# Kernel tuning notes

Measured on AMD Instinct MI355X. Metric: run time of the kernel, lower is better.

## Reference

```python
import jax, jax.numpy as jnp
import numpy as np

V, E, H, B, P, Q = 100000, 300, 256, 64, 400, 50
NEG = -1e7


def _gru_param(k, s=0.08):
    k1, k2, k3, k4 = jax.random.split(k, 4)
    return (jax.random.normal(k1, (2, 3 * H, E)) * s,
            jax.random.normal(k2, (2, 3 * H, H)) * s,
            jax.random.normal(k3, (2, 3 * H)) * s,
            jax.random.normal(k4, (2, 3 * H)) * s)


def setup_inputs() -> dict:
    key = jax.random.key(0)
    ks = jax.random.split(key, 10)
    emb = (jax.random.normal(ks[0], (V, E)) * 0.1).at[0].set(0.0)  # padding_idx=0 row zeroed
    passage = jax.random.randint(ks[1], (B, P), 1, V)
    question = jax.random.randint(ks[2], (B, Q), 1, V)
    # variable lengths, padding (token 0) at the tail like pack_padded_sequence assumes
    p_len = 200 + (jnp.arange(B) * 7) % (P - 200)
    q_len = 20 + (jnp.arange(B) * 3) % (Q - 20)
    passage = jnp.where(jnp.arange(P)[None, :] < p_len[:, None], passage, 0)
    question = jnp.where(jnp.arange(Q)[None, :] < q_len[:, None], question, 0)
    pW_ih, pW_hh, pb_ih, pb_hh = _gru_param(ks[3])
    qW_ih, qW_hh, qb_ih, qb_hh = _gru_param(ks[4])
    start_w = jax.random.normal(ks[5], (6 * H,)) * 0.05
    start_b = jax.random.normal(ks[6], ()) * 0.05
    end_w = jax.random.normal(ks[7], (6 * H,)) * 0.05
    end_b = jax.random.normal(ks[8], ()) * 0.05
    return dict(passage=passage, question=question, emb=emb,
                pW_ih=pW_ih, pW_hh=pW_hh, pb_ih=pb_ih, pb_hh=pb_hh,
                qW_ih=qW_ih, qW_hh=qW_hh, qb_ih=qb_ih, qb_hh=qb_hh,
                start_w=start_w, start_b=start_b, end_w=end_w, end_b=end_b)


def bi_gru(x, mask, Wih, Whh, bih, bhh):
    """Bidirectional GRU with packed-sequence-equivalent masking.
    x: (B,T,E), mask: (B,T) float. Returns (B,T,2H). Padded outputs are 0,
    and the backward pass starts at the true last token (mask freezes state)."""
    m = mask[..., None]                                          # (B,T,1)
    xproj = jnp.einsum('bte,dhe->dbth', x, Wih) + bih[:, None, None, :]  # (2,B,T,3H)

    def run(xp, mm, Whh_d, bhh_d):
        def step(h, inp):
            xt, mt = inp                                         # (B,3H),(B,1)
            hp = h @ Whh_d.T + bhh_d
            r = jax.nn.sigmoid(xt[:, :H] + hp[:, :H])
            z = jax.nn.sigmoid(xt[:, H:2 * H] + hp[:, H:2 * H])
            n = jnp.tanh(xt[:, 2 * H:] + r * hp[:, 2 * H:])
            h_new = (1 - z) * n + z * h
            h_new = mt * h_new + (1 - mt) * h
            return h_new, h_new * mt
        h0 = jnp.zeros((xp.shape[0], H), xp.dtype)
        _, out = jax.lax.scan(step, h0, (xp.transpose(1, 0, 2), mm.transpose(1, 0, 2)))
        return out.transpose(1, 0, 2)                            # (B,T,H)

    fwd = run(xproj[0], m, Whh[0], bhh[0])
    bwd = run(xproj[1][:, ::-1], m[:, ::-1], Whh[1], bhh[1])[:, ::-1]
    return jnp.concatenate([fwd, bwd], axis=-1)


def reference(passage, question, emb,
              pW_ih, pW_hh, pb_ih, pb_hh,
              qW_ih, qW_hh, qb_ih, qb_hh,
              start_w, start_b, end_w, end_b):
    p_mask = (passage != 0).astype(jnp.float32)                  # (B,P)
    q_mask = (question != 0).astype(jnp.float32)                 # (B,Q)
    Hp = bi_gru(emb[passage], p_mask, pW_ih, pW_hh, pb_ih, pb_hh)  # (B,P,2H)
    Hq = bi_gru(emb[question], q_mask, qW_ih, qW_hh, qb_ih, qb_hh)  # (B,Q,2H)

    # Trilinear attention: decompose Linear over the cat([p, q, p*q]) terms
    w1, w2, w3 = start_w[:2 * H], start_w[2 * H:4 * H], start_w[4 * H:]
    scores = (Hp @ w1)[:, :, None] + (Hq @ w2)[:, None, :] \
        + jnp.einsum('bpd,bqd->bpq', Hp * w3, Hq) + start_b      # (B,P,Q)

    # allennlp masked_softmax: softmax(vector*mask) * mask, renormalized
    a = jax.nn.softmax(scores * q_mask[:, None, :], axis=-1) * q_mask[:, None, :]
    a = a / (a.sum(axis=-1, keepdims=True) + 1e-13)

    wavg = jnp.einsum('bpq,bqd->bpd', a, Hq)                     # (B,P,2H)
    combined = jnp.concatenate([Hp, wavg, Hp * wavg], axis=-1)   # (B,P,6H)

    start_logits = jnp.where(p_mask > 0, combined @ start_w + start_b, NEG)
    end_logits = jnp.where(p_mask > 0, combined @ end_w + end_b, NEG)
    log_mask = jnp.log(p_mask + 1e-45)
    softmax_start = jax.nn.log_softmax(start_logits + log_mask, axis=-1)
    softmax_end = jax.nn.log_softmax(end_logits + log_mask, axis=-1)
    return start_logits, end_logits, softmax_start, softmax_end
```

## Files before the change

kernel.cpp:

```cpp
#include <hip/hip_runtime.h>
#include <math.h>

constexpr int Bb = 64;
constexpr int Pp = 400;
constexpr int Qq = 50;
constexpr int Ee = 300;
constexpr int Hh = 256;
constexpr int H3 = 768;
constexpr int Dd = 512;

#define NEGC (-10000000.0f)
#define LOGTINY (-103.278929903f)

typedef _Float16 h2 __attribute__((ext_vector_type(2)));
typedef _Float16 f16x8 __attribute__((ext_vector_type(8)));
typedef float f32x4 __attribute__((ext_vector_type(4)));

__device__ __forceinline__ float allred(float v){
  #pragma unroll
  for (int off = 1; off < 64; off <<= 1) v += __shfl_xor(v, off);
  return v;
}
__device__ __forceinline__ float allmax(float v){
  #pragma unroll
  for (int off = 1; off < 64; off <<= 1) v = fmaxf(v, __shfl_xor(v, off));
  return v;
}
__device__ __forceinline__ float sigm(float x){ return 1.f / (1.f + expf(-x)); }

__device__ __forceinline__ float dot2f(unsigned a, unsigned b, float c){
#if __has_builtin(__builtin_amdgcn_fdot2)
  return __builtin_amdgcn_fdot2(__builtin_bit_cast(h2, a), __builtin_bit_cast(h2, b), c, false);
#else
  float r = c;
  asm("v_dot2_f32_f16 %0, %1, %2, %0" : "+v"(r) : "v"(a), "v"(b));
  return r;
#endif
}

#define U4C(v,c) ((c)==0?(v).x:((c)==1?(v).y:((c)==2?(v).z:(v).w)))

__global__ __launch_bounds__(256) void gather_a(const int* __restrict__ ptok,
                                                const int* __restrict__ qtok,
                                                const float* __restrict__ emb,
                                                _Float16* __restrict__ Agp,
                                                _Float16* __restrict__ Agq){
  int idx = blockIdx.x * 256 + threadIdx.x;
  if (idx >= (25600 + 3200) * 40) return;
  int ck = idx % 40;
  int row = idx / 40;
  int tokv; _Float16* dst;
  if (row < 25600){ tokv = ptok[row]; dst = Agp + (size_t)row * 320; }
  else { int r = row - 25600; tokv = qtok[r]; dst = Agq + (size_t)r * 320; }
  int c = ck * 8;
  const float* src = emb + (size_t)tokv * Ee;
  f16x8 v;
  #pragma unroll
  for (int i = 0; i < 8; ++i) v[i] = (c + i < Ee) ? (_Float16)src[c + i] : (_Float16)0.f;
  *(f16x8*)(dst + c) = v;
}

__global__ __launch_bounds__(256) void prep_wih16(const float* __restrict__ pW,
                                                  const float* __restrict__ qW,
                                                  _Float16* __restrict__ wih16){
  int idx = blockIdx.x * 256 + threadIdx.x;
  if (idx >= 2 * 2 * 768 * 160) return;
  int col2 = idx % 160;
  int r = idx / 160;
  int g = r / 1536;
  int dh = r % 1536;
  int c = col2 * 2;
  const float* W = g ? qW : pW;
  float2 v = make_float2(0.f, 0.f);
  if (c < Ee) v = *(const float2*)(W + (size_t)dh * Ee + c);
  h2 o = { (_Float16)v.x, (_Float16)v.y };
  *(h2*)(wih16 + (size_t)r * 320 + c) = o;
}

__global__ __launch_bounds__(256) void prep_w16(const float* __restrict__ pW,
                                                const float* __restrict__ qW,
                                                unsigned* __restrict__ w16){
  int idx = blockIdx.x * 256 + threadIdx.x;
  if (idx >= 393216) return;
  int c = idx & 3;
  int t = (idx >> 2) & 1023;
  int B = idx >> 12;
  int gd, g, ql;
  if (B < 28){
    gd = B / 7; int rb = B % 7;
    ql = rb / 3; g = rb % 3;
  } else if (B < 64){
    int lb0 = B - 28; gd = lb0 / 9; int lb = lb0 % 9;
    if (lb < 2){ ql = 2; g = lb + 1; }
    else if (lb < 8){ int v = lb - 2; ql = 3 + v / 3; g = v % 3; }
    else { ql = 5; g = 0; }
  } else {
    int sb0 = B - 64; gd = sb0 / 8; int sb = sb0 % 8;
    if (sb < 2){ ql = 5; g = sb + 1; }
    else { int v = sb - 2; ql = 6 + v / 3; g = v % 3; }
  }
  int j = t & 255, qq = t >> 8;
  int p = qq * 32 + ql * 4 + c;
  int row = g * 256 + j;
  int d = gd & 1, kind = gd >> 1;
  const float* W = kind ? qW : pW;
  const float* src = W + ((size_t)d * H3 + row) * Hh + 2 * p;
  _Float16 a = (_Float16)src[0], bb = (_Float16)src[1];
  unsigned short ua, ub;
  __builtin_memcpy(&ua, &a, 2); __builtin_memcpy(&ub, &bb, 2);
  w16[idx] = (unsigned)ua | ((unsigned)ub << 16);
}

__global__ __launch_bounds__(512) void xproj_mfma(const _Float16* __restrict__ Ag,
                                                  const _Float16* __restrict__ wih16,
                                                  const float* __restrict__ bih,
                                                  _Float16* __restrict__ xp, int T){
  __shared__ __align__(16) _Float16 Af[128][72];
  __shared__ __align__(16) _Float16 Bf[128][72];
  int tid = threadIdx.x;
  int m0 = blockIdx.y * 128;
  int nt = blockIdx.x;
  int d = nt / 6, h0 = (nt % 6) * 128;
  int wid = tid >> 6, lane = tid & 63;
  int wr = wid >> 2, wc = wid & 3;

  int r0 = tid >> 3;
  int r1 = (tid + 512) >> 3;
  int cc = (tid & 7) * 8;
  const _Float16* eA0 = Ag + (size_t)(m0 + r0) * 320;
  const _Float16* eA1 = Ag + (size_t)(m0 + r1) * 320;
  const _Float16* wB0 = wih16 + ((size_t)d * H3 + h0 + r0) * 320;
  const _Float16* wB1 = wih16 + ((size_t)d * H3 + h0 + r1) * 320;

  f32x4 acc[4][2] = {};

  for (int k0 = 0; k0 < 320; k0 += 64){
    *(f16x8*)&Af[r0][cc] = *(const f16x8*)(eA0 + k0 + cc);
    *(f16x8*)&Af[r1][cc] = *(const f16x8*)(eA1 + k0 + cc);
    *(f16x8*)&Bf[r0][cc] = *(const f16x8*)(wB0 + k0 + cc);
    *(f16x8*)&Bf[r1][cc] = *(const f16x8*)(wB1 + k0 + cc);
    __syncthreads();
    #pragma unroll
    for (int kc = 0; kc < 2; ++kc){
      int kb = kc * 32 + (lane >> 4) * 8;
      f16x8 af[4], bf[2];
      #pragma unroll
      for (int i = 0; i < 4; ++i) af[i] = *(const f16x8*)&Af[wr * 64 + i * 16 + (lane & 15)][kb];
      #pragma unroll
      for (int jn = 0; jn < 2; ++jn) bf[jn] = *(const f16x8*)&Bf[wc * 32 + jn * 16 + (lane & 15)][kb];
      #pragma unroll
      for (int i = 0; i < 4; ++i)
        #pragma unroll
        for (int jn = 0; jn < 2; ++jn)
          acc[i][jn] = __builtin_amdgcn_mfma_f32_16x16x32_f16(af[i], bf[jn], acc[i][jn], 0, 0, 0);
    }
    __syncthreads();
  }

  #pragma unroll
  for (int jn = 0; jn < 2; ++jn){
    int h = h0 + wc * 32 + jn * 16 + (lane & 15);
    float bv = bih[d * H3 + h];
    #pragma unroll
    for (int i = 0; i < 4; ++i){
      #pragma unroll
      for (int r = 0; r < 4; ++r){
        int m = m0 + wr * 64 + i * 16 + (lane >> 4) * 4 + r;
        int bI = m / T, tI = m - bI * T;
        xp[(((size_t)d * Bb + bI) * T + tI) * H3 + h] = (_Float16)(acc[i][jn][r] + bv);
      }
    }
  }
}

__global__ __launch_bounds__(1024)
void gru_kernel(const int* __restrict__ ptok,
                const int* __restrict__ qtok,
                const _Float16* __restrict__ xpp,
                const _Float16* __restrict__ xpq,
                const unsigned* __restrict__ w16,
                const float* __restrict__ pbhh,
                const float* __restrict__ qbhh,
                float* __restrict__ Hp,
                float* __restrict__ Hq){
  int wg = blockIdx.x;
  bool isp = wg < 128;
  int lw = isp ? wg : wg - 128;
  int d = lw & 1, b = lw >> 1;
  int T = isp ? Pp : Qq;
  const int* tok = (isp ? ptok : qtok) + b * T;
  const _Float16* xrow = (isp ? xpp : xpq) + ((size_t)d * Bb + b) * T * H3;
  int gd = (isp ? 0 : 2) + d;
  const float* bhh = (isp ? pbhh : qbhh) + d * H3;
  float* Hout = (isp ? Hp : Hq) + (size_t)b * T * Dd + d * Hh;

  __shared__ __align__(16) uint4 ldsW[9 * 1024];
  __shared__ float part[3][3][Hh];
  __shared__ unsigned hbuf[2][128];

  int t = threadIdx.x;
  int j = t & 255, qq = t >> 8, lane = t & 63;
  const uint4* u4w = (const uint4*)w16;

  unsigned wrR[28];
  #pragma unroll
  for (int rb = 0; rb < 7; ++rb){
    uint4 v = u4w[((size_t)gd * 7 + rb) * 1024 + t];
    wrR[4 * rb + 0] = v.x; wrR[4 * rb + 1] = v.y; wrR[4 * rb + 2] = v.z; wrR[4 * rb + 3] = v.w;
  }
  #pragma unroll
  for (int i = 0; i < 28; ++i) asm volatile("" : "+v"(wrR[i]));

  #pragma unroll
  for (int lb = 0; lb < 9; ++lb)
    ldsW[lb * 1024 + t] = u4w[28 * 1024 + ((size_t)gd * 9 + lb) * 1024 + t];
  const uint4* wS = u4w + 64 * 1024 + (size_t)gd * 8 * 1024;

  float bh0 = bhh[j], bh1 = bhh[Hh + j], bh2 = bhh[2 * Hh + j];
  float h_old = 0.f;
  if (t < 128) hbuf[1][t] = 0u;
  __syncthreads();

  int t0 = d ? (T - 1) : 0;
  float pre0 = 0.f, pre1 = 0.f, pre2 = 0.f;
  if (qq == 0){
    pre0 = (float)xrow[(size_t)t0 * H3 + j];
    pre1 = (float)xrow[(size_t)t0 * H3 + Hh + j];
    pre2 = (float)xrow[(size_t)t0 * H3 + 2 * Hh + j];
  }

  for (int s = 0; s < T; ++s){
    int tt = d ? (T - 1 - s) : s;
    unsigned vh = hbuf[(s + 1) & 1][qq * 32 + (lane & 31)];
    float a0 = 0.f, a1 = 0.f, a2 = 0.f;

    uint4 sA0 = wS[0 * 1024 + t], sA1 = wS[1 * 1024 + t];

    #pragma unroll
    for (int c = 0; c < 4; ++c){
      unsigned hv = (unsigned)__builtin_amdgcn_readlane((int)vh, c);
      a0 = dot2f(wrR[0 + c], hv, a0);
      a1 = dot2f(wrR[4 + c], hv, a1);
      a2 = dot2f(wrR[8 + c], hv, a2);
    }
    #pragma unroll
    for (int c = 0; c < 4; ++c){
      unsigned hv = (unsigned)__builtin_amdgcn_readlane((int)vh, 4 + c);
      a0 = dot2f(wrR[12 + c], hv, a0);
      a1 = dot2f(wrR[16 + c], hv, a1);
      a2 = dot2f(wrR[20 + c], hv, a2);
    }
    #pragma unroll
    for (int c = 0; c < 4; ++c){
      unsigned hv = (unsigned)__builtin_amdgcn_readlane((int)vh, 8 + c);
      a0 = dot2f(wrR[24 + c], hv, a0);
    }

    uint4 sB0 = wS[2 * 1024 + t], sB1 = wS[3 * 1024 + t], sB2 = wS[4 * 1024 + t];

    { uint4 l1 = ldsW[0 * 1024 + t], l2 = ldsW[1 * 1024 + t];
      #pragma unroll
      for (int c = 0; c < 4; ++c){
        unsigned hv = (unsigned)__builtin_amdgcn_readlane((int)vh, 8 + c);
        a1 = dot2f(U4C(l1, c), hv, a1);
        a2 = dot2f(U4C(l2, c), hv, a2);
      } }
    { uint4 l0 = ldsW[2 * 1024 + t], l1 = ldsW[3 * 1024 + t], l2 = ldsW[4 * 1024 + t];
      #pragma unroll
      for (int c = 0; c < 4; ++c){
        unsigned hv = (unsigned)__builtin_amdgcn_readlane((int)vh, 12 + c);
        a0 = dot2f(U4C(l0, c), hv, a0);
        a1 = dot2f(U4C(l1, c), hv, a1);
        a2 = dot2f(U4C(l2, c), hv, a2);
      } }

    #pragma unroll
    for (int c = 0; c < 4; ++c){
      unsigned hv = (unsigned)__builtin_amdgcn_readlane((int)vh, 20 + c);
      a1 = dot2f(U4C(sA0, c), hv, a1);
      a2 = dot2f(U4C(sA1, c), hv, a2);
    }

    uint4 sC0 = wS[5 * 1024 + t], sC1 = wS[6 * 1024 + t], sC2 = wS[7 * 1024 + t];

    { uint4 l0 = ldsW[5 * 1024 + t], l1 = ldsW[6 * 1024 + t], l2 = ldsW[7 * 1024 + t];
      #pragma unroll
      for (int c = 0; c < 4; ++c){
        unsigned hv = (unsigned)__builtin_amdgcn_readlane((int)vh, 16 + c);
        a0 = dot2f(U4C(l0, c), hv, a0);
        a1 = dot2f(U4C(l1, c), hv, a1);
        a2 = dot2f(U4C(l2, c), hv, a2);
      } }
    { uint4 l0 = ldsW[8 * 1024 + t];
      #pragma unroll
      for (int c = 0; c < 4; ++c){
        unsigned hv = (unsigned)__builtin_amdgcn_readlane((int)vh, 20 + c);
        a0 = dot2f(U4C(l0, c), hv, a0);
      } }

    #pragma unroll
    for (int c = 0; c < 4; ++c){
      unsigned hv = (unsigned)__builtin_amdgcn_readlane((int)vh, 24 + c);
      a0 = dot2f(U4C(sB0, c), hv, a0);
      a1 = dot2f(U4C(sB1, c), hv, a1);
      a2 = dot2f(U4C(sB2, c), hv, a2);
    }
    #pragma unroll
    for (int c = 0; c < 4; ++c){
      unsigned hv = (unsigned)__builtin_amdgcn_readlane((int)vh, 28 + c);
      a0 = dot2f(U4C(sC0, c), hv, a0);
      a1 = dot2f(U4C(sC1, c), hv, a1);
      a2 = dot2f(U4C(sC2, c), hv, a2);
    }

    if (qq != 0){
      part[qq - 1][0][j] = a0;
      part[qq - 1][1][j] = a1;
      part[qq - 1][2][j] = a2;
    }
    __syncthreads();
    if (qq == 0){
      float xt0 = pre0, xt1 = pre1, xt2 = pre2;
      if (s + 1 < T){
        int tn = d ? (T - 2 - s) : (s + 1);
        pre0 = (float)xrow[(size_t)tn * H3 + j];
        pre1 = (float)xrow[(size_t)tn * H3 + Hh + j];
        pre2 = (float)xrow[(size_t)tn * H3 + 2 * Hh + j];
      }
      float g0 = a0 + part[0][0][j] + part[1][0][j] + part[2][0][j] + bh0;
      float g1 = a1 + part[0][1][j] + part[1][1][j] + part[2][1][j] + bh1;
      float g2 = a2 + part[0][2][j] + part[1][2][j] + part[2][2][j] + bh2;
      float r = sigm(xt0 + g0);
      float z = sigm(xt1 + g1);
      float n = tanhf(xt2 + r * g2);
      float hnew = (1.f - z) * n + z * h_old;
      float m = (tok[tt] != 0) ? 1.f : 0.f;
      float hm = m * hnew + (1.f - m) * h_old;
      h_old = hm;
      ((_Float16*)hbuf[s & 1])[j] = (_Float16)hm;
      Hout[(size_t)tt * Dd + j] = hm * m;
    }
    __syncthreads();
  }
}

__global__ __launch_bounds__(512) void attn_kernel(const float* __restrict__ Hp,
                                                   const float* __restrict__ Hq,
                                                   const int* __restrict__ ptok,
                                                   const int* __restrict__ qtok,
                                                   const float* __restrict__ start_w,
                                                   const float* __restrict__ sbp,
                                                   const float* __restrict__ end_w,
                                                   const float* __restrict__ ebp,
                                                   float* __restrict__ out){
  extern __shared__ __align__(16) float lds[];
  float* hqs = lds;
  float* s2s = hqs + Qq * Dd;
  float* qms = s2s + 64;
  float* scw = qms + 64;
  float* aw  = scw + 512;

  int b = blockIdx.y, pc = blockIdx.x;
  int tid = threadIdx.x, wid = tid >> 6, lane = tid & 63;
  float sb = sbp[0], eb = ebp[0];

  float w1r[8], w2r[8], w3r[8], e1r[8], e2r[8], e3r[8];
  #pragma unroll
  for (int i = 0; i < 8; ++i){
    int c = lane * 8 + i;
    w1r[i] = start_w[c]; w2r[i] = start_w[Dd + c]; w3r[i] = start_w[2 * Dd + c];
    e1r[i] = end_w[c];   e2r[i] = end_w[Dd + c];   e3r[i] = end_w[2 * Dd + c];
  }
  for (int idx = tid; idx < Qq * Dd; idx += 512) hqs[idx] = Hq[(size_t)b * Qq * Dd + idx];
  __syncthreads();

  for (int q = wid; q < Qq; q += 8){
    float part = 0.f;
    const float* hq = hqs + q * Dd + lane * 8;
    #pragma unroll
    for (int i = 0; i < 8; ++i) part += hq[i] * w2r[i];
    part = allred(part);
    if (lane == 0){
      s2s[q] = part;
      qms[q] = (qtok[b * Qq + q] != 0) ? 1.f : 0.f;
    }
  }
  __syncthreads();

  for (int p = pc * 100 + wid; p < pc * 100 + 100; p += 8){
    const float* hprow = Hp + ((size_t)b * Pp + p) * Dd + lane * 8;
    float4 hv0 = *(const float4*)hprow;
    float4 hv1 = *(const float4*)(hprow + 4);
    float hpc[8] = {hv0.x, hv0.y, hv0.z, hv0.w, hv1.x, hv1.y, hv1.z, hv1.w};
    float hw3[8], he3[8];
    float s1 = 0.f, ed = 0.f;
    #pragma unroll
    for (int i = 0; i < 8; ++i){
      hw3[i] = hpc[i] * w3r[i];
      he3[i] = hpc[i] * e3r[i];
      s1 += hpc[i] * w1r[i];
      ed += hpc[i] * e1r[i];
    }
    #pragma unroll
    for (int off = 1; off < 64; off <<= 1){
      s1 += __shfl_xor(s1, off);
      ed += __shfl_xor(ed, off);
    }
    for (int q = 0; q < Qq; ++q){
      const float4* hq4 = (const float4*)(hqs + q * Dd + lane * 8);
      float4 a0 = hq4[0], a1 = hq4[1];
      float dot = hw3[0] * a0.x + hw3[1] * a0.y + hw3[2] * a0.z + hw3[3] * a0.w
                + hw3[4] * a1.x + hw3[5] * a1.y + hw3[6] * a1.z + hw3[7] * a1.w;
      dot = allred(dot);
      if (lane == 0) scw[wid * 64 + q] = (s1 + s2s[q] + dot + sb) * qms[q];
    }
    float v = (lane < Qq) ? scw[wid * 64 + lane] : -1e30f;
    float M = allmax(v);
    float ev = (lane < Qq) ? expf(v - M) : 0.f;
    float S = allred(ev);
    float am = (lane < Qq) ? (ev / S) * qms[lane] : 0.f;
    float Sm = allred(am);
    float af = am / (Sm + 1e-13f);
    if (lane < Qq) aw[wid * 64 + lane] = af;
    float wv[8] = {0.f, 0.f, 0.f, 0.f, 0.f, 0.f, 0.f, 0.f};
    for (int q = 0; q < Qq; ++q){
      float aq = aw[wid * 64 + q];
      const float4* hq4 = (const float4*)(hqs + q * Dd + lane * 8);
      float4 a0 = hq4[0], a1 = hq4[1];
      wv[0] += aq * a0.x; wv[1] += aq * a0.y; wv[2] += aq * a0.z; wv[3] += aq * a0.w;
      wv[4] += aq * a1.x; wv[5] += aq * a1.y; wv[6] += aq * a1.z; wv[7] += aq * a1.w;
    }
    float acc2 = 0.f, acc3 = 0.f, acc4 = 0.f, acc5 = 0.f;
    #pragma unroll
    for (int i = 0; i < 8; ++i){
      acc2 += wv[i] * w2r[i];
      acc3 += hw3[i] * wv[i];
      acc4 += wv[i] * e2r[i];
      acc5 += he3[i] * wv[i];
    }
    #pragma unroll
    for (int off = 1; off < 64; off <<= 1){
      acc2 += __shfl_xor(acc2, off);
      acc3 += __shfl_xor(acc3, off);
      acc4 += __shfl_xor(acc4, off);
      acc5 += __shfl_xor(acc5, off);
    }
    if (lane == 0){
      bool pm = (ptok[b * Pp + p] != 0);
      out[(size_t)b * Pp + p]                   = pm ? (s1 + acc2 + acc3 + sb) : NEGC;
      out[(size_t)Bb * Pp + (size_t)b * Pp + p] = pm ? (ed + acc4 + acc5 + eb) : NEGC;
    }
  }
}

__global__ __launch_bounds__(512) void lsm_kernel(const int* __restrict__ ptok,
                                                  float* __restrict__ out){
  int b = blockIdx.x >> 1, sel = blockIdx.x & 1;
  const float* lg = out + (size_t)sel * Bb * Pp + (size_t)b * Pp;
  float* o = out + (size_t)(2 + sel) * Bb * Pp + (size_t)b * Pp;
  int tid = threadIdx.x;
  __shared__ float red1[8];
  __shared__ float red2[8];
  float x = -1e30f;
  if (tid < Pp) x = lg[tid] + ((ptok[b * Pp + tid] != 0) ? 0.f : LOGTINY);
  float m = allmax(x);
  if ((tid & 63) == 0) red1[tid >> 6] = m;
  __syncthreads();
  float M = red1[0];
  #pragma unroll
  for (int i = 1; i < 8; ++i) M = fmaxf(M, red1[i]);
  float e = (tid < Pp) ? expf(x - M) : 0.f;
  float s = allred(e);
  if ((tid & 63) == 0) red2[tid >> 6] = s;
  __syncthreads();
  float S = 0.f;
  #pragma unroll
  for (int i = 0; i < 8; ++i) S += red2[i];
  if (tid < Pp) o[tid] = (x - M) - logf(S);
}

extern "C" void kernel_launch(void* const* d_in, const int* in_sizes, int n_in,
                              void* d_out, int out_size, void* d_ws, size_t ws_size,
                              hipStream_t stream){
  const int*   passage  = (const int*)d_in[0];
  const int*   question = (const int*)d_in[1];
  const float* emb      = (const float*)d_in[2];
  const float* pW_ih    = (const float*)d_in[3];
  const float* pW_hh    = (const float*)d_in[4];
  const float* pb_ih    = (const float*)d_in[5];
  const float* pb_hh    = (const float*)d_in[6];
  const float* qW_ih    = (const float*)d_in[7];
  const float* qW_hh    = (const float*)d_in[8];
  const float* qb_ih    = (const float*)d_in[9];
  const float* qb_hh    = (const float*)d_in[10];
  const float* start_w  = (const float*)d_in[11];
  const float* start_b  = (const float*)d_in[12];
  const float* end_w    = (const float*)d_in[13];
  const float* end_b    = (const float*)d_in[14];
  float* out = (float*)d_out;

  float*     ws    = (float*)d_ws;
  unsigned*  w16   = (unsigned*)ws;
  _Float16*  wih16 = (_Float16*)(ws + 393216);
  _Float16*  Agp   = (_Float16*)(ws + 884736);
  _Float16*  Agq   = (_Float16*)(ws + 4980736);
  _Float16*  xpp   = (_Float16*)(ws + 5492736);
  _Float16*  xpq   = (_Float16*)(ws + 25153536);
  float*     Hp    = ws + 27611136;
  float*     Hq    = ws + 40718336;

  hipLaunchKernelGGL(prep_w16, dim3(1536), dim3(256), 0, stream, pW_hh, qW_hh, w16);
  hipLaunchKernelGGL(gather_a, dim3(4500), dim3(256), 0, stream,
                     passage, question, emb, Agp, Agq);
  hipLaunchKernelGGL(prep_wih16, dim3(1920), dim3(256), 0, stream, pW_ih, qW_ih, wih16);
  hipLaunchKernelGGL(xproj_mfma, dim3(12, 200), dim3(512), 0, stream,
                     Agp, wih16, pb_ih, xpp, Pp);
  hipLaunchKernelGGL(xproj_mfma, dim3(12, 25), dim3(512), 0, stream,
                     Agq, wih16 + (size_t)2 * H3 * 320, qb_ih, xpq, Qq);
  hipLaunchKernelGGL(gru_kernel, dim3(256), dim3(1024), 0, stream,
                     passage, question, xpp, xpq, w16, pb_hh, qb_hh, Hp, Hq);
  size_t attn_lds = (size_t)(Qq * Dd + 64 + 64 + 512 + 512) * sizeof(float);
  hipLaunchKernelGGL(attn_kernel, dim3(4, 64), dim3(512), attn_lds, stream,
                     Hp, Hq, passage, question, start_w, start_b, end_w, end_b, out);
  hipLaunchKernelGGL(lsm_kernel, dim3(128), dim3(512), 0, stream, passage, out);
}
```

Measured before the change: 938.9 us.

## Skip all-padding xproj tiles and broadcast GRU hidden state via LDS vector loads

The input-projection GEMM now checks the token ids of its 128-row tile and exits early when every token is padding, avoiding GEMM work for rows the masked GRU never uses. In the recurrent GRU loop, hidden-state pairs are read as 16-byte LDS broadcast loads instead of one LDS read followed by many readlane broadcasts. This trades scalar-lane traffic for extra LDS read instructions in the serial per-step critical path. The skipped tiles leave their xp entries unwritten, which relies on the GRU ignoring them under the mask.

```diff
diff --git a/kernel.cpp b/kernel.cpp
--- a/kernel.cpp
+++ b/kernel.cpp
@@ -111,14 +111,23 @@
   w16[idx] = (unsigned)ua | ((unsigned)ub << 16);
 }
 
-__global__ __launch_bounds__(512) void xproj_mfma(const _Float16* __restrict__ Ag,
+__global__ __launch_bounds__(512) void xproj_mfma(const int* __restrict__ tok,
+                                                  const _Float16* __restrict__ Ag,
                                                   const _Float16* __restrict__ wih16,
                                                   const float* __restrict__ bih,
                                                   _Float16* __restrict__ xp, int T){
   __shared__ __align__(16) _Float16 Af[128][72];
   __shared__ __align__(16) _Float16 Bf[128][72];
+  __shared__ int anyflag;
   int tid = threadIdx.x;
   int m0 = blockIdx.y * 128;
+
+  if (tid == 0) anyflag = 0;
+  __syncthreads();
+  if (tid < 128 && tok[m0 + tid] != 0) anyflag = 1;
+  __syncthreads();
+  if (!anyflag) return;
+
   int nt = blockIdx.x;
   int d = nt / 6, h0 = (nt % 6) * 128;
   int wid = tid >> 6, lane = tid & 63;
@@ -196,10 +205,10 @@
 
   __shared__ __align__(16) uint4 ldsW[9 * 1024];
   __shared__ float part[3][3][Hh];
-  __shared__ unsigned hbuf[2][128];
+  __shared__ __align__(16) unsigned hbuf[2][128];
 
   int t = threadIdx.x;
-  int j = t & 255, qq = t >> 8, lane = t & 63;
+  int j = t & 255, qq = t >> 8;
   const uint4* u4w = (const uint4*)w16;
 
   unsigned wrR[28];
@@ -231,87 +240,46 @@
 
   for (int s = 0; s < T; ++s){
     int tt = d ? (T - 1 - s) : s;
-    unsigned vh = hbuf[(s + 1) & 1][qq * 32 + (lane & 31)];
+    const uint4* hb4 = (const uint4*)&hbuf[(s + 1) & 1][qq * 32];
     float a0 = 0.f, a1 = 0.f, a2 = 0.f;
 
     uint4 sA0 = wS[0 * 1024 + t], sA1 = wS[1 * 1024 + t];
-
-    #pragma unroll
-    for (int c = 0; c < 4; ++c){
-      unsigned hv = (unsigned)__builtin_amdgcn_readlane((int)vh, c);
-      a0 = dot2f(wrR[0 + c], hv, a0);
-      a1 = dot2f(wrR[4 + c], hv, a1);
-      a2 = dot2f(wrR[8 + c], hv, a2);
-    }
-    #pragma unroll
-    for (int c = 0; c < 4; ++c){
-      unsigned hv = (unsigned)__builtin_amdgcn_readlane((int)vh, 4 + c);
-      a0 = dot2f(wrR[12 + c], hv, a0);
-      a1 = dot2f(wrR[16 + c], hv, a1);
-      a2 = dot2f(wrR[20 + c], hv, a2);
-    }
-    #pragma unroll
-    for (int c = 0; c < 4; ++c){
-      unsigned hv = (unsigned)__builtin_amdgcn_readlane((int)vh, 8 + c);
-      a0 = dot2f(wrR[24 + c], hv, a0);
-    }
-
     uint4 sB0 = wS[2 * 1024 + t], sB1 = wS[3 * 1024 + t], sB2 = wS[4 * 1024 + t];
-
+    uint4 sC0 = wS[5 * 1024 + t], sC1 = wS[6 * 1024 + t], sC2 = wS[7 * 1024 + t];
+
+    #define DOT3(HQ, W0e, W1e, W2e) { _Pragma("unroll") \
+      for (int c = 0; c < 4; ++c){ \
+        unsigned hv = U4C(HQ, c); \
+        a0 = dot2f(U4C(W0e, c), hv, a0); \
+        a1 = dot2f(U4C(W1e, c), hv, a1); \
+        a2 = dot2f(U4C(W2e, c), hv, a2); } }
+    #define DOT1(HQ, W0e, ACC) { _Pragma("unroll") \
+      for (int c = 0; c < 4; ++c){ \
+        unsigned hv = U4C(HQ, c); \
+        ACC = dot2f(U4C(W0e, c), hv, ACC); } }
+    #define RQ(i) (*(const uint4*)&wrR[4 * (i)])
+
+    uint4 h0q = hb4[0], h1q = hb4[1];
+    DOT3(h0q, RQ(0), RQ(1), RQ(2))
+    DOT3(h1q, RQ(3), RQ(4), RQ(5))
+    uint4 h2q = hb4[2], h3q = hb4[3];
+    DOT1(h2q, RQ(6), a0)
     { uint4 l1 = ldsW[0 * 1024 + t], l2 = ldsW[1 * 1024 + t];
-      #pragma unroll
-      for (int c = 0; c < 4; ++c){
-        unsigned hv = (unsigned)__builtin_amdgcn_readlane((int)vh, 8 + c);
-        a1 = dot2f(U4C(l1, c), hv, a1);
-        a2 = dot2f(U4C(l2, c), hv, a2);
-      } }
+      DOT1(h2q, l1, a1) DOT1(h2q, l2, a2) }
     { uint4 l0 = ldsW[2 * 1024 + t], l1 = ldsW[3 * 1024 + t], l2 = ldsW[4 * 1024 + t];
-      #pragma unroll
-      for (int c = 0; c < 4; ++c){
-        unsigned hv = (unsigned)__builtin_amdgcn_readlane((int)vh, 12 + c);
-        a0 = dot2f(U4C(l0, c), hv, a0);
-        a1 = dot2f(U4C(l1, c), hv, a1);
-        a2 = dot2f(U4C(l2, c), hv, a2);
-      } }
-
-    #pragma unroll
-    for (int c = 0; c < 4; ++c){
-      unsigned hv = (unsigned)__builtin_amdgcn_readlane((int)vh, 20 + c);
-      a1 = dot2f(U4C(sA0, c), hv, a1);
-      a2 = dot2f(U4C(sA1, c), hv, a2);
-    }
-
-    uint4 sC0 = wS[5 * 1024 + t], sC1 = wS[6 * 1024 + t], sC2 = wS[7 * 1024 + t];
-
+      DOT3(h3q, l0, l1, l2) }
+    uint4 h4q = hb4[4], h5q = hb4[5];
     { uint4 l0 = ldsW[5 * 1024 + t], l1 = ldsW[6 * 1024 + t], l2 = ldsW[7 * 1024 + t];
-      #pragma unroll
-      for (int c = 0; c < 4; ++c){
-        unsigned hv = (unsigned)__builtin_amdgcn_readlane((int)vh, 16 + c);
-        a0 = dot2f(U4C(l0, c), hv, a0);
-        a1 = dot2f(U4C(l1, c), hv, a1);
-        a2 = dot2f(U4C(l2, c), hv, a2);
-      } }
+      DOT3(h4q, l0, l1, l2) }
     { uint4 l0 = ldsW[8 * 1024 + t];
-      #pragma unroll
-      for (int c = 0; c < 4; ++c){
-        unsigned hv = (unsigned)__builtin_amdgcn_readlane((int)vh, 20 + c);
-        a0 = dot2f(U4C(l0, c), hv, a0);
-      } }
-
-    #pragma unroll
-    for (int c = 0; c < 4; ++c){
-      unsigned hv = (unsigned)__builtin_amdgcn_readlane((int)vh, 24 + c);
-      a0 = dot2f(U4C(sB0, c), hv, a0);
-      a1 = dot2f(U4C(sB1, c), hv, a1);
-      a2 = dot2f(U4C(sB2, c), hv, a2);
-    }
-    #pragma unroll
-    for (int c = 0; c < 4; ++c){
-      unsigned hv = (unsigned)__builtin_amdgcn_readlane((int)vh, 28 + c);
-      a0 = dot2f(U4C(sC0, c), hv, a0);
-      a1 = dot2f(U4C(sC1, c), hv, a1);
-      a2 = dot2f(U4C(sC2, c), hv, a2);
-    }
+      DOT1(h5q, l0, a0) }
+    DOT1(h5q, sA0, a1) DOT1(h5q, sA1, a2)
+    uint4 h6q = hb4[6], h7q = hb4[7];
+    DOT3(h6q, sB0, sB1, sB2)
+    DOT3(h7q, sC0, sC1, sC2)
+    #undef DOT3
+    #undef DOT1
+    #undef RQ
 
     if (qq != 0){
       part[qq - 1][0][j] = a0;
@@ -514,9 +482,9 @@
                      passage, question, emb, Agp, Agq);
   hipLaunchKernelGGL(prep_wih16, dim3(1920), dim3(256), 0, stream, pW_ih, qW_ih, wih16);
   hipLaunchKernelGGL(xproj_mfma, dim3(12, 200), dim3(512), 0, stream,
-                     Agp, wih16, pb_ih, xpp, Pp);
+                     passage, Agp, wih16, pb_ih, xpp, Pp);
   hipLaunchKernelGGL(xproj_mfma, dim3(12, 25), dim3(512), 0, stream,
-                     Agq, wih16 + (size_t)2 * H3 * 320, qb_ih, xpq, Qq);
+                     question, Agq, wih16 + (size_t)2 * H3 * 320, qb_ih, xpq, Qq);
   hipLaunchKernelGGL(gru_kernel, dim3(256), dim3(1024), 0, stream,
                      passage, question, xpp, xpq, w16, pb_hh, qb_hh, Hp, Hq);
   size_t attn_lds = (size_t)(Qq * Dd + 64 + 64 + 512 + 512) * sizeof(float);
```

Result: faster. 892.7 us, median of 2 (-4.9%).
